# Performance work log

Measured on AMD Instinct MI355X. Metric: run time of the kernel, lower is better.

The kernel has to match this reference:

```python
import jax, jax.numpy as jnp
import numpy as np

KAPPA = 1.0
SIGMA = 0.3
EPS = 1e-5  # torch BatchNorm1d default eps


def _bn(y, g, b):
    # training-mode batch norm: biased batch statistics over the batch axis
    mu = jnp.mean(y, axis=0)
    var = jnp.mean((y - mu) ** 2, axis=0)
    return g * (y - mu) * jax.lax.rsqrt(var + EPS) + b


def _hid(x, W, b, g, be):
    # Linear -> BatchNorm1d -> ReLU
    return jax.nn.relu(_bn(x @ W + b, g, be))


def setup_inputs() -> dict:
    key = jax.random.key(0)
    ks = jax.random.split(key, 12)
    B, D, H, T = 2048, 256, 266, 51  # H = dim + 10
    S = T - 1
    sc = jnp.float32(0.1)
    f32 = jnp.float32
    inp = {}
    inp["x"] = jax.random.normal(ks[0], (B, D), f32)
    inp["dW"] = jax.random.normal(ks[1], (S, B, D), f32)   # hoisted per-step noise xi
    inp["law"] = jax.random.normal(ks[2], (S, D), f32)
    inp["timegrid"] = jnp.linspace(0.0, 1.0, T).astype(f32)
    # per-timestep MLP stacks (i_h1 / h1_h2 / h2_o)
    inp["W1"] = sc * jax.random.normal(ks[3], (S, D, H), f32)
    inp["b1"] = jnp.zeros((S, H), f32)
    inp["g1"] = jnp.ones((S, H), f32)
    inp["be1"] = jnp.zeros((S, H), f32)
    inp["W2"] = sc * jax.random.normal(ks[4], (S, H, H), f32)
    inp["b2"] = jnp.zeros((S, H), f32)
    inp["g2"] = jnp.ones((S, H), f32)
    inp["be2"] = jnp.zeros((S, H), f32)
    inp["W3"] = sc * jax.random.normal(ks[5], (S, H, D), f32)
    inp["b3"] = jnp.zeros((S, D), f32)
    # v0 network (v0_i_h1 / v0_h1_h2 / v0_h2_o, all Linear+BN+ReLU)
    inp["Wv1"] = sc * jax.random.normal(ks[6], (D, H), f32)
    inp["bv1"] = jnp.zeros((H,), f32)
    inp["gv1"] = jnp.ones((H,), f32)
    inp["bev1"] = jnp.zeros((H,), f32)
    inp["Wv2"] = sc * jax.random.normal(ks[7], (H, H), f32)
    inp["bv2"] = jnp.zeros((H,), f32)
    inp["gv2"] = jnp.ones((H,), f32)
    inp["bev2"] = jnp.zeros((H,), f32)
    inp["Wv3"] = sc * jax.random.normal(ks[8], (H, 1), f32)
    inp["bv3"] = jnp.zeros((1,), f32)
    inp["gv3"] = jnp.ones((1,), f32)
    inp["bev3"] = jnp.zeros((1,), f32)
    return inp


def reference(x, dW, law, timegrid,
              W1, b1, g1, be1, W2, b2, g2, be2, W3, b3,
              Wv1, bv1, gv1, bev1, Wv2, bv2, gv2, bev2, Wv3, bv3, gv3, bev3):
    hgrid = jnp.diff(timegrid)  # [S]
    # v0 network evaluated on the initial state (note: last stage is also Linear+BN+ReLU)
    v0 = _hid(_hid(_hid(x, Wv1, bv1, gv1, bev1), Wv2, bv2, gv2, bev2), Wv3, bv3, gv3, bev3)  # [B,1]

    def step(carry, xs):
        xc, v = carry
        w1, bb1, gg1, bbe1, w2, bb2, gg2, bbe2, w3, bb3, li, dw, h = xs
        h1 = _hid(xc, w1, bb1, gg1, bbe1)
        h2 = _hid(h1, w2, bb2, gg2, bbe2)
        grad = h2 @ w3 + bb3                                   # [B,D]
        # f = kappa^2/2 * ||x - law_i||^2 + 1/2 * ||alpha||^2,  alpha = -grad
        f = 0.5 * KAPPA ** 2 * jnp.sum((xc - li) ** 2, axis=1) + 0.5 * jnp.sum(grad ** 2, axis=1)
        noise = SIGMA * jnp.sqrt(h) * dw                       # [B,D]
        # diag(grad @ noise^T) == rowwise dot product: O(B*D) instead of O(B^2*D)
        v = v - (f * h)[:, None] + jnp.sum(grad * noise, axis=1, keepdims=True)
        xc = xc - grad * h + noise
        return (xc, v), None

    (x_final, v), _ = jax.lax.scan(
        step, (x, v0),
        (W1, b1, g1, be1, W2, b2, g2, be2, W3, b3, law, dW, hgrid))
    return v  # [B,1]; (x_final and the path are byproducts of the same scan)
```

## Files before the change

### kernel.cpp

```cpp
#include <hip/hip_runtime.h>
#include <hip/hip_bf16.h>


#define BATCH 2048
#define DD    256
#define HH    266
#define HP    272
#define SS    50
#define BN_EPS 1e-5f
#define SIG   0.3f
#define AS_STRIDE 296
#define YS    276
#define XS    260

#define V_OFF  1638400
#define S1_OFF 1640448
#define S2_OFF 1649152
#define S1V_OFF 1657856
#define S2V_OFF 1662208
#define SV_OFF  1666560
#define WQ_OFF  1666576

#define W1S 69632
#define W2S 78336
#define W3S 73728
#define W1Q_OFF 0
#define W2Q_OFF 3481600
#define W3Q_OFF 7398400
#define WV1Q_OFF 11084800
#define WV2Q_OFF 11154432

#define BAR_OFF 7283200

typedef unsigned short ushort_t;
using short8 = __attribute__((ext_vector_type(8))) short;
using f32x4  = __attribute__((ext_vector_type(4))) float;
using f32x2  = __attribute__((ext_vector_type(2))) float;

__device__ __forceinline__ ushort_t f2b(float f) {
    unsigned u = __float_as_uint(f);
    unsigned r = u + 0x7FFF + ((u >> 16) & 1);
    return (ushort_t)(r >> 16);
}

__device__ __forceinline__ float ld_coh(const float* p) {
    return __hip_atomic_load((const float*)p, __ATOMIC_RELAXED, __HIP_MEMORY_SCOPE_AGENT);
}
__device__ __forceinline__ f32x2 ld2_coh(const float* p) {
    f32x2 v;
    asm volatile("global_load_dwordx2 %0, %1, off sc0 sc1" : "=v"(v) : "v"(p));
    return v;
}

__global__ __launch_bounds__(256) void k_conv(const float* __restrict__ src,
                                              ushort_t* __restrict__ dst,
                                              int K, int N, int KT, int NT,
                                              long total) {
    long t = (long)blockIdx.x * 256 + threadIdx.x;
    if (t >= total) return;
    int per = KT * NT * 512;
    int step = (int)(t / per);
    int e = (int)(t - (long)step * per);
    int kt = e / (NT * 512);
    int r = e - kt * NT * 512;
    int nt = r / 512;
    int r2 = r & 511;
    int lane = r2 >> 3;
    int j = r2 & 7;
    int k = kt * 32 + (lane >> 4) * 8 + j;
    int n = nt * 16 + (lane & 15);
    float v = (k < K && n < N) ? src[(size_t)step * K * N + (size_t)k * N + n] : 0.f;
    dst[t] = f2b(v);
}

__global__ __launch_bounds__(256) void k_pre(float* __restrict__ ws) {
    unsigned* bar = (unsigned*)(ws + BAR_OFF);
    for (int i = threadIdx.x; i < 768; i += 256) atomicExch(bar + i, 0u);
}

__device__ __forceinline__ void grid_bar(unsigned* bar, unsigned gen, int bid) {
    (void)bid;
    __syncthreads();
    if (threadIdx.x == 0) {
        unsigned* cnt = bar;
        unsigned* rel = bar + 32;
        unsigned a = __hip_atomic_fetch_add(cnt, 1u, __ATOMIC_RELAXED, __HIP_MEMORY_SCOPE_AGENT);
        if (a == gen * 128u + 127u) {
            __hip_atomic_store(rel, gen + 1u, __ATOMIC_RELAXED, __HIP_MEMORY_SCOPE_AGENT);
        } else {
            while (__hip_atomic_load(rel, __ATOMIC_RELAXED, __HIP_MEMORY_SCOPE_AGENT) < gen + 1u)
                __builtin_amdgcn_s_sleep(1);
        }
        asm volatile("" ::: "memory");
    }
    __syncthreads();
}

__device__ __forceinline__ void compute_ac_coh(const float* __restrict__ si,
                                               const float* __restrict__ g,
                                               const float* __restrict__ be,
                                               float (*AC)[HP]) {
    int t = threadIdx.x;
    if (t < 136) {
        f32x2 sv[8], qv[8];
        #pragma unroll
        for (int r = 0; r < 8; ++r) {
            sv[r] = ld2_coh(si + r * 544 + 2 * t);
            qv[r] = ld2_coh(si + r * 544 + 272 + 2 * t);
        }
        asm volatile("s_waitcnt vmcnt(0)" ::: "memory");
        __builtin_amdgcn_sched_barrier(0);
        f32x2 s = sv[0], q = qv[0];
        #pragma unroll
        for (int r = 1; r < 8; ++r) { s += sv[r]; q += qv[r]; }
        #pragma unroll
        for (int j = 0; j < 2; ++j) {
            int col = 2 * t + j;
            float a = 0.f, c = 0.f;
            if (col < HH) {
                float mu  = s[j] * (1.0f / 2048.0f);
                float var = q[j] * (1.0f / 2048.0f) - mu * mu;
                float rs  = rsqrtf(fmaxf(var, 0.0f) + BN_EPS);
                a = g[col] * rs;
                c = be[col] - mu * a;
            }
            AC[0][col] = a;
            AC[1][col] = c;
        }
    }
}

__device__ __forceinline__ void dev_lin16(
    int bid, int mode, int KT,
    const float* __restrict__ gsrc, const float* __restrict__ lsrc,
    const float* __restrict__ stats_in, const float* __restrict__ g,
    const float* __restrict__ be,
    const ushort_t* __restrict__ Wq, const float* __restrict__ bias,
    float* __restrict__ ylds, float* __restrict__ stats_out,
    float* __restrict__ zero_ptr,
    const float* __restrict__ pfd, const float* __restrict__ pfl,
    const float* __restrict__ pfb,
    ushort_t* __restrict__ As, float (*AC)[HP])
{
    const int tid  = threadIdx.x;
    const int lane = tid & 63;
    const int wv   = tid >> 6;
    const int quad = lane >> 4;
    const int l15  = lane & 15;
    const int row0 = bid * 16;

    f32x4 pv0 = {0.f,0.f,0.f,0.f}, pv1 = {0.f,0.f,0.f,0.f}, pv2 = {0.f,0.f,0.f,0.f};
    if (pfd != nullptr) {
        pv0 = ((const f32x4*)pfd)[tid];
        pv1 = ((const f32x4*)pfd)[tid + 512];
        if (tid < 64)        pv2 = ((const f32x4*)pfl)[tid];
        else if (tid < 128)  pv2 = ((const f32x4*)pfb)[tid - 64];
    }

    if (zero_ptr != nullptr) {
        int z = bid * 512 + tid;
        if (z < 4352) atomicExch(zero_ptr + z, 0.0f);
    }

    if (mode == 2) { compute_ac_coh(stats_in, g, be, AC); __syncthreads(); }

    const int PAIRS = KT * 16;
    for (int idx = tid; idx < 16 * PAIRS; idx += 512) {
        int m  = idx / PAIRS;
        int kk = (idx - m * PAIRS) * 2;
        float v0, v1;
        if (mode == 2) {
            v0 = (kk < HH)   ? fmaxf(fmaf(AC[0][kk],   lsrc[m * YS + kk],   AC[1][kk]),   0.f) : 0.f;
            v1 = (kk+1 < HH) ? fmaxf(fmaf(AC[0][kk+1], lsrc[m * YS + kk+1], AC[1][kk+1]), 0.f) : 0.f;
        } else {
            v0 = gsrc[(size_t)(row0 + m) * DD + kk];
            v1 = gsrc[(size_t)(row0 + m) * DD + kk + 1];
        }
        ((unsigned int*)As)[m * (AS_STRIDE/2) + (kk >> 1)] =
            (unsigned int)f2b(v0) | ((unsigned int)f2b(v1) << 16);
    }
    if (pfd != nullptr) {
        asm volatile("" :: "v"(pv0), "v"(pv1));
        if (tid < 128) asm volatile("" :: "v"(pv2));
    }
    __syncthreads();

    f32x4 acc[3];
    #pragma unroll
    for (int i = 0; i < 3; ++i) acc[i] = (f32x4){0.f, 0.f, 0.f, 0.f};

    #pragma unroll 3
    for (int kt = 0; kt < KT; ++kt) {
        short8 af = *(const short8*)(&As[l15 * AS_STRIDE + kt * 32 + quad * 8]);
        const ushort_t* wp = Wq + ((size_t)(kt * 17 + wv)) * 512 + lane * 8;
        #pragma unroll
        for (int i = 0; i < 3; ++i) {
            if (i < 2 || wv == 0) {
                short8 bf = *(const short8*)(wp + (size_t)i * 8 * 512);
                acc[i] = __builtin_amdgcn_mfma_f32_16x16x32_bf16(af, bf, acc[i], 0, 0, 0);
            }
        }
    }

    #pragma unroll
    for (int i = 0; i < 3; ++i) {
        if (i == 2 && wv != 0) continue;
        int t = wv + 8 * i;
        int col = t * 16 + l15;
        float bj = (col < HH) ? bias[col] : 0.f;
        float y0 = acc[i][0] + bj, y1 = acc[i][1] + bj;
        float y2 = acc[i][2] + bj, y3 = acc[i][3] + bj;
        ylds[(quad*4 + 0) * YS + col] = y0;
        ylds[(quad*4 + 1) * YS + col] = y1;
        ylds[(quad*4 + 2) * YS + col] = y2;
        ylds[(quad*4 + 3) * YS + col] = y3;
        float sp = y0 + y1 + y2 + y3;
        float sq = y0*y0 + y1*y1 + y2*y2 + y3*y3;
        sp += __shfl_xor(sp, 16); sp += __shfl_xor(sp, 32);
        sq += __shfl_xor(sq, 16); sq += __shfl_xor(sq, 32);
        if (quad == 0 && col < HH) {
            float* spp = stats_out + (bid & 7) * 544;
            atomicAdd(spp + col, sp);
            atomicAdd(spp + 272 + col, sq);
        }
    }
}

__device__ __forceinline__ void dev_fused16(
    int bid,
    const float* __restrict__ y2l, const float* __restrict__ stats_in,
    const float* __restrict__ g2, const float* __restrict__ be2,
    const ushort_t* __restrict__ W3q, const float* __restrict__ b3,
    const float* __restrict__ law, const float* __restrict__ dWs,
    const float* __restrict__ tg, int s, int doP1,
    float* __restrict__ xcl, float* __restrict__ vv, float* __restrict__ outv,
    const ushort_t* __restrict__ W1q, const float* __restrict__ b1n,
    float* __restrict__ y1l, float* __restrict__ stats_out,
    float* __restrict__ zero_ptr,
    ushort_t* __restrict__ As, float (*AC)[HP], float* __restrict__ red)
{
    const int tid  = threadIdx.x;
    const int lane = tid & 63;
    const int wv   = tid >> 6;
    const int quad = lane >> 4;
    const int l15  = lane & 15;
    const int row0 = bid * 16;

    if (zero_ptr != nullptr) {
        int z = bid * 512 + tid;
        if (z < 4352) atomicExch(zero_ptr + z, 0.0f);
    }

    compute_ac_coh(stats_in, g2, be2, AC);
    __syncthreads();

    for (int idx = tid; idx < 16 * 144; idx += 512) {
        int m  = idx / 144;
        int kk = (idx - m * 144) * 2;
        float v0 = (kk < HH)   ? fmaxf(fmaf(AC[0][kk],   y2l[m * YS + kk],   AC[1][kk]),   0.f) : 0.f;
        float v1 = (kk+1 < HH) ? fmaxf(fmaf(AC[0][kk+1], y2l[m * YS + kk+1], AC[1][kk+1]), 0.f) : 0.f;
        ((unsigned int*)As)[m * (AS_STRIDE/2) + (kk >> 1)] =
            (unsigned int)f2b(v0) | ((unsigned int)f2b(v1) << 16);
    }
    __syncthreads();

    f32x4 acc[2];
    acc[0] = (f32x4){0.f,0.f,0.f,0.f};
    acc[1] = (f32x4){0.f,0.f,0.f,0.f};
    #pragma unroll 3
    for (int kt = 0; kt < 9; ++kt) {
        short8 af = *(const short8*)(&As[l15 * AS_STRIDE + kt * 32 + quad * 8]);
        const ushort_t* wp = W3q + ((size_t)(kt * 16 + wv)) * 512 + lane * 8;
        acc[0] = __builtin_amdgcn_mfma_f32_16x16x32_bf16(af, *(const short8*)(wp),           acc[0], 0, 0, 0);
        acc[1] = __builtin_amdgcn_mfma_f32_16x16x32_bf16(af, *(const short8*)(wp + 8 * 512), acc[1], 0, 0, 0);
    }

    const float h   = tg[s + 1] - tg[s];
    const float srt = SIG * sqrtf(h);
    float grad[2][4], xcv[2][4], dwv[2][4];
    float sxr[4], sgr[4], sgnr[4];
    #pragma unroll
    for (int i = 0; i < 2; ++i) {
        int col = (wv + 8*i) * 16 + l15;
        const float lawv = law[col];
        const float b3v  = b3[col];
        #pragma unroll
        for (int r = 0; r < 4; ++r) {
            int rl = quad * 4 + r;
            float gd = acc[i][r] + b3v;
            float xv = xcl[rl * XS + col];
            float dw = dWs[(size_t)(row0 + rl) * DD + col];
            float d  = xv - lawv;
            grad[i][r] = gd; xcv[i][r] = xv; dwv[i][r] = dw;
            if (i == 0) {
                sxr[r]  = d * d;
                sgr[r]  = gd * gd;
                sgnr[r] = gd * dw;
            } else {
                sxr[r]  = fmaf(d, d, sxr[r]);
                sgr[r]  = fmaf(gd, gd, sgr[r]);
                sgnr[r] = fmaf(gd, dw, sgnr[r]);
            }
        }
    }
    #pragma unroll
    for (int off = 1; off < 16; off <<= 1) {
        #pragma unroll
        for (int r = 0; r < 4; ++r) {
            sxr[r]  += __shfl_xor(sxr[r],  off);
            sgr[r]  += __shfl_xor(sgr[r],  off);
            sgnr[r] += __shfl_xor(sgnr[r], off);
        }
    }
    if (l15 == 0) {
        #pragma unroll
        for (int r = 0; r < 4; ++r) {
            int rr = quad * 4 + r;
            red[(wv * 16 + rr) * 3 + 0] = sxr[r];
            red[(wv * 16 + rr) * 3 + 1] = sgr[r];
            red[(wv * 16 + rr) * 3 + 2] = sgnr[r];
        }
    }
    __syncthreads();

    if (tid < 16) {
        float sx = 0.f, sg = 0.f, sgn = 0.f;
        #pragma unroll
        for (int w = 0; w < 8; ++w) {
            sx  += red[(w * 16 + tid) * 3 + 0];
            sg  += red[(w * 16 + tid) * 3 + 1];
            sgn += red[(w * 16 + tid) * 3 + 2];
        }
        int row = row0 + tid;
        float f  = 0.5f * (sx + sg);
        float vn = vv[row] - f * h + srt * sgn;
        vv[row] = vn;
        if (s == SS - 1) outv[row] = vn;
    }

    #pragma unroll
    for (int i = 0; i < 2; ++i) {
        int col = (wv + 8*i) * 16 + l15;
        #pragma unroll
        for (int r = 0; r < 4; ++r) {
            int rl = quad * 4 + r;
            float xn = xcv[i][r] - grad[i][r] * h + srt * dwv[i][r];
            xcl[rl * XS + col] = xn;
            if (doP1) As[rl * AS_STRIDE + col] = f2b(xn);
        }
    }
    if (!doP1) return;
    __syncthreads();

    f32x4 acc2[3];
    #pragma unroll
    for (int i = 0; i < 3; ++i) acc2[i] = (f32x4){0.f, 0.f, 0.f, 0.f};
    #pragma unroll 4
    for (int kt = 0; kt < 8; ++kt) {
        short8 af = *(const short8*)(&As[l15 * AS_STRIDE + kt * 32 + quad * 8]);
        const ushort_t* wp = W1q + ((size_t)(kt * 17 + wv)) * 512 + lane * 8;
        #pragma unroll
        for (int i = 0; i < 3; ++i) {
            if (i < 2 || wv == 0) {
                short8 bf = *(const short8*)(wp + (size_t)i * 8 * 512);
                acc2[i] = __builtin_amdgcn_mfma_f32_16x16x32_bf16(af, bf, acc2[i], 0, 0, 0);
            }
        }
    }
    #pragma unroll
    for (int i = 0; i < 3; ++i) {
        if (i == 2 && wv != 0) continue;
        int t = wv + 8 * i;
        int col = t * 16 + l15;
        float bj = (col < HH) ? b1n[col] : 0.f;
        float y0 = acc2[i][0] + bj, y1 = acc2[i][1] + bj;
        float y2 = acc2[i][2] + bj, y3 = acc2[i][3] + bj;
        y1l[(quad*4 + 0) * YS + col] = y0;
        y1l[(quad*4 + 1) * YS + col] = y1;
        y1l[(quad*4 + 2) * YS + col] = y2;
        y1l[(quad*4 + 3) * YS + col] = y3;
        float sp = y0 + y1 + y2 + y3;
        float sq = y0*y0 + y1*y1 + y2*y2 + y3*y3;
        sp += __shfl_xor(sp, 16); sp += __shfl_xor(sp, 32);
        sq += __shfl_xor(sq, 16); sq += __shfl_xor(sq, 32);
        if (quad == 0 && col < HH) {
            float* spp = stats_out + (bid & 7) * 544;
            atomicAdd(spp + col, sp);
            atomicAdd(spp + 272 + col, sq);
        }
    }
}

__device__ __forceinline__ void dev_v0l3_16(
    int bid, const float* __restrict__ y2l, const float* __restrict__ stats_in,
    const float* __restrict__ gv, const float* __restrict__ bev,
    const float* __restrict__ wv3, const float* __restrict__ bv3,
    float* __restrict__ vout, float* __restrict__ sv,
    float (*AC)[HP], float* __restrict__ xtra)
{
    const int tid = threadIdx.x;
    compute_ac_coh(stats_in, gv, bev, AC);
    __syncthreads();

    const int r  = tid >> 5;
    const int ks = tid & 31;
    int k0 = ks * 9, k1 = k0 + 9;
    if (k1 > HH) k1 = HH;
    float acc = 0.0f;
    for (int k = k0; k < k1; ++k) {
        float y  = y2l[r * YS + k];
        float a2 = fmaxf(fmaf(AC[0][k], y, AC[1][k]), 0.0f);
        acc = fmaf(a2, wv3[k], acc);
    }
    #pragma unroll
    for (int off = 1; off < 32; off <<= 1) acc += __shfl_xor(acc, off);
    if (ks == 0) {
        float y = acc + bv3[0];
        vout[bid * 16 + r] = y;
        xtra[r] = y;
        xtra[16 + r] = y * y;
    }
    __syncthreads();
    if (tid == 0) {
        float s = 0.f, q = 0.f;
        #pragma unroll
        for (int i = 0; i < 16; ++i) { s += xtra[i]; q += xtra[16 + i]; }
        atomicAdd(sv, s);
        atomicAdd(sv + 1, q);
    }
}

__device__ __forceinline__ void dev_v0fin16(int bid, float* __restrict__ v,
                                            const float* __restrict__ sv,
                                            const float* __restrict__ gv3,
                                            const float* __restrict__ bev3) {
    if (threadIdx.x < 16) {
        float s0 = ld_coh(sv);
        float s1 = ld_coh(sv + 1);
        float mu  = s0 * (1.0f / 2048.0f);
        float var = s1 * (1.0f / 2048.0f) - mu * mu;
        float rs  = rsqrtf(fmaxf(var, 0.0f) + BN_EPS);
        int row = bid * 16 + threadIdx.x;
        float y = v[row];
        v[row] = fmaxf(gv3[0] * (y - mu) * rs + bev3[0], 0.0f);
    }
}

__global__ __launch_bounds__(512) void k_persist(
    const float* __restrict__ x, const float* __restrict__ dW,
    const float* __restrict__ law, const float* __restrict__ tg,
    const float* __restrict__ b1, const float* __restrict__ g1, const float* __restrict__ be1,
    const float* __restrict__ b2, const float* __restrict__ g2, const float* __restrict__ be2,
    const float* __restrict__ b3,
    const float* __restrict__ bv1, const float* __restrict__ gv1, const float* __restrict__ bev1,
    const float* __restrict__ bv2, const float* __restrict__ gv2, const float* __restrict__ bev2,
    const float* __restrict__ Wv3, const float* __restrict__ bv3,
    const float* __restrict__ gv3, const float* __restrict__ bev3,
    float* __restrict__ ws, float* __restrict__ out)
{
    __shared__ ushort_t As[16 * AS_STRIDE];
    __shared__ float AC[2][HP];
    __shared__ float Y1s[16 * YS];
    __shared__ float Y2s[16 * YS];
    __shared__ float XCs[16 * XS];
    __shared__ float XTRA[384];

    const int bid = blockIdx.x;
    const int tid = threadIdx.x;

    float* V   = ws + V_OFF;
    float* S1  = ws + S1_OFF;
    float* S2  = ws + S2_OFF;
    float* S1v = ws + S1V_OFF;
    float* S2v = ws + S2V_OFF;
    float* SV  = ws + SV_OFF;
    ushort_t* WQ = (ushort_t*)(ws + WQ_OFF);
    ushort_t* W1q  = WQ + W1Q_OFF;
    ushort_t* W2q  = WQ + W2Q_OFF;
    ushort_t* W3q  = WQ + W3Q_OFF;
    ushort_t* Wv1q = WQ + WV1Q_OFF;
    ushort_t* Wv2q = WQ + WV2Q_OFF;
    unsigned* bar  = (unsigned*)(ws + BAR_OFF);

    unsigned gen = 0;

    for (int i = tid; i < 16 * DD; i += 512) {
        int r = i >> 8, c = i & 255;
        XCs[r * XS + c] = x[(size_t)bid * 16 * DD + i];
    }
    {
        int z = bid * 512 + tid;
        if (z < 26128) atomicExch(S1 + z, 0.0f);
    }
    grid_bar(bar, gen, bid); gen++;

    dev_lin16(bid, 0, 8, x, nullptr, nullptr, nullptr, nullptr,
              Wv1q, bv1, Y1s, S1v, nullptr, nullptr, nullptr, nullptr, As, AC);
    grid_bar(bar, gen, bid); gen++;

    dev_lin16(bid, 2, 9, nullptr, Y1s, S1v, gv1, bev1,
              Wv2q, bv2, Y2s, S2v, nullptr, nullptr, nullptr, nullptr, As, AC);
    grid_bar(bar, gen, bid); gen++;

    dev_v0l3_16(bid, Y2s, S2v, gv2, bev2, Wv3, bv3, V, SV, AC, XTRA);
    grid_bar(bar, gen, bid); gen++;

    dev_v0fin16(bid, V, SV, gv3, bev3);
    dev_lin16(bid, 0, 8, x, nullptr, nullptr, nullptr, nullptr,
              W1q, b1, Y1s, S1, nullptr, nullptr, nullptr, nullptr, As, AC);
    grid_bar(bar, gen, bid); gen++;

    for (int s = 0; s < SS; ++s) {
        int p = s & 1;
        dev_lin16(bid, 2, 9, nullptr, Y1s, S1 + p * 4352,
                  g1 + s * HH, be1 + s * HH,
                  W2q + (size_t)s * W2S, b2 + s * HH,
                  Y2s, S2 + p * 4352, S1 + (1 - p) * 4352,
                  dW + (size_t)s * BATCH * DD + (size_t)bid * 16 * DD,
                  law + (size_t)s * DD, b3 + (size_t)s * DD, As, AC);
        grid_bar(bar, gen, bid); gen++;

        int sn = (s + 1 < SS) ? s + 1 : 0;
        dev_fused16(bid, Y2s, S2 + p * 4352,
                    g2 + s * HH, be2 + s * HH,
                    W3q + (size_t)s * W3S, b3 + s * DD,
                    law + s * DD, dW + (size_t)s * BATCH * DD,
                    tg, s, (s < SS - 1) ? 1 : 0,
                    XCs, V, out,
                    W1q + (size_t)sn * W1S, b1 + sn * HH,
                    Y1s, S1 + ((s + 1) & 1) * 4352,
                    S2 + (1 - p) * 4352, As, AC, XTRA);
        grid_bar(bar, gen, bid); gen++;
    }
}

extern "C" void kernel_launch(void* const* d_in, const int* in_sizes, int n_in,
                              void* d_out, int out_size, void* d_ws, size_t ws_size,
                              hipStream_t stream)
{
    (void)in_sizes; (void)n_in; (void)out_size; (void)ws_size;
    const float* x    = (const float*)d_in[0];
    const float* dW   = (const float*)d_in[1];
    const float* law  = (const float*)d_in[2];
    const float* tg   = (const float*)d_in[3];
    const float* W1   = (const float*)d_in[4];
    const float* b1   = (const float*)d_in[5];
    const float* g1   = (const float*)d_in[6];
    const float* be1  = (const float*)d_in[7];
    const float* W2   = (const float*)d_in[8];
    const float* b2   = (const float*)d_in[9];
    const float* g2   = (const float*)d_in[10];
    const float* be2  = (const float*)d_in[11];
    const float* W3   = (const float*)d_in[12];
    const float* b3   = (const float*)d_in[13];
    const float* Wv1  = (const float*)d_in[14];
    const float* bv1  = (const float*)d_in[15];
    const float* gv1  = (const float*)d_in[16];
    const float* bev1 = (const float*)d_in[17];
    const float* Wv2  = (const float*)d_in[18];
    const float* bv2  = (const float*)d_in[19];
    const float* gv2  = (const float*)d_in[20];
    const float* bev2 = (const float*)d_in[21];
    const float* Wv3  = (const float*)d_in[22];
    const float* bv3  = (const float*)d_in[23];
    const float* gv3  = (const float*)d_in[24];
    const float* bev3 = (const float*)d_in[25];

    float* ws = (float*)d_ws;
    ushort_t* WQ = (ushort_t*)(ws + WQ_OFF);
    ushort_t* W1q  = WQ + W1Q_OFF;
    ushort_t* W2q  = WQ + W2Q_OFF;
    ushort_t* W3q  = WQ + W3Q_OFF;
    ushort_t* Wv1q = WQ + WV1Q_OFF;
    ushort_t* Wv2q = WQ + WV2Q_OFF;
    float* out = (float*)d_out;

    k_pre<<<1, 256, 0, stream>>>(ws);
    k_conv<<<13600, 256, 0, stream>>>(W1,  W1q,  DD, HH, 8, 17, (long)SS * W1S);
    k_conv<<<15300, 256, 0, stream>>>(W2,  W2q,  HH, HH, 9, 17, (long)SS * W2S);
    k_conv<<<14400, 256, 0, stream>>>(W3,  W3q,  HH, DD, 9, 16, (long)SS * W3S);
    k_conv<<<272,   256, 0, stream>>>(Wv1, Wv1q, DD, HH, 8, 17, (long)W1S);
    k_conv<<<306,   256, 0, stream>>>(Wv2, Wv2q, HH, HH, 9, 17, (long)W2S);

    k_persist<<<128, 512, 0, stream>>>(
        x, dW, law, tg,
        b1, g1, be1, b2, g2, be2, b3,
        bv1, gv1, bev1, bv2, gv2, bev2,
        Wv3, bv3, gv3, bev3,
        ws, out);
}
```

Baseline: 1.458 ms.

## Use hierarchical grid barrier and prefetch next-stage weights before barriers

Replaces the single-counter grid barrier with a two-level tree: 8 leaf counters of 16 blocks each, a root counter, and per-leaf release flags, so the 128 blocks no longer contend on one atomic. Prefetches move to just before each barrier and now cover the block's 16-row slice of dW, law and b3, plus a 1/16 slice of the next W3, W1 and W2 bf16 weights, to warm L2 while blocks wait. Zeroing of the stats buffers is spread as small per-block chunks instead of being done by the first few blocks. The gain depends on barrier latency and L2 hit rates, and the two-level barrier adds an extra atomic hop on the critical path.

```diff
diff --git a/kernel.cpp b/kernel.cpp
--- a/kernel.cpp
+++ b/kernel.cpp
@@ -50,6 +50,13 @@
     f32x2 v;
     asm volatile("global_load_dwordx2 %0, %1, off sc0 sc1" : "=v"(v) : "v"(p));
     return v;
+}
+__device__ __forceinline__ void pf2(const f32x4* q, int n, int tid,
+                                    f32x4& r0, f32x4& r1) {
+    int i0 = (tid < n) ? tid : 0;
+    int i1 = (tid + 512 < n) ? (tid + 512) : 0;
+    r0 = q[i0];
+    r1 = q[i1];
 }
 
 __global__ __launch_bounds__(256) void k_conv(const float* __restrict__ src,
@@ -79,15 +86,24 @@
 }
 
 __device__ __forceinline__ void grid_bar(unsigned* bar, unsigned gen, int bid) {
-    (void)bid;
     __syncthreads();
     if (threadIdx.x == 0) {
-        unsigned* cnt = bar;
-        unsigned* rel = bar + 32;
-        unsigned a = __hip_atomic_fetch_add(cnt, 1u, __ATOMIC_RELAXED, __HIP_MEMORY_SCOPE_AGENT);
-        if (a == gen * 128u + 127u) {
-            __hip_atomic_store(rel, gen + 1u, __ATOMIC_RELAXED, __HIP_MEMORY_SCOPE_AGENT);
-        } else {
+        const int lf = bid & 7;
+        unsigned* leaf = bar + lf * 32;
+        unsigned* root = bar + 256;
+        unsigned* rel  = bar + 288 + lf * 32;
+        bool done = false;
+        unsigned a = __hip_atomic_fetch_add(leaf, 1u, __ATOMIC_RELAXED, __HIP_MEMORY_SCOPE_AGENT);
+        if (a == gen * 16u + 15u) {
+            unsigned r = __hip_atomic_fetch_add(root, 1u, __ATOMIC_RELAXED, __HIP_MEMORY_SCOPE_AGENT);
+            if (r == gen * 8u + 7u) {
+                #pragma unroll
+                for (int l = 0; l < 8; ++l)
+                    __hip_atomic_store(bar + 288 + l * 32, gen + 1u, __ATOMIC_RELAXED, __HIP_MEMORY_SCOPE_AGENT);
+                done = true;
+            }
+        }
+        if (!done) {
             while (__hip_atomic_load(rel, __ATOMIC_RELAXED, __HIP_MEMORY_SCOPE_AGENT) < gen + 1u)
                 __builtin_amdgcn_s_sleep(1);
         }
@@ -138,8 +154,6 @@
     const ushort_t* __restrict__ Wq, const float* __restrict__ bias,
     float* __restrict__ ylds, float* __restrict__ stats_out,
     float* __restrict__ zero_ptr,
-    const float* __restrict__ pfd, const float* __restrict__ pfl,
-    const float* __restrict__ pfb,
     ushort_t* __restrict__ As, float (*AC)[HP])
 {
     const int tid  = threadIdx.x;
@@ -149,18 +163,8 @@
     const int l15  = lane & 15;
     const int row0 = bid * 16;
 
-    f32x4 pv0 = {0.f,0.f,0.f,0.f}, pv1 = {0.f,0.f,0.f,0.f}, pv2 = {0.f,0.f,0.f,0.f};
-    if (pfd != nullptr) {
-        pv0 = ((const f32x4*)pfd)[tid];
-        pv1 = ((const f32x4*)pfd)[tid + 512];
-        if (tid < 64)        pv2 = ((const f32x4*)pfl)[tid];
-        else if (tid < 128)  pv2 = ((const f32x4*)pfb)[tid - 64];
-    }
-
-    if (zero_ptr != nullptr) {
-        int z = bid * 512 + tid;
-        if (z < 4352) atomicExch(zero_ptr + z, 0.0f);
-    }
+    if (zero_ptr != nullptr && tid < 34)
+        atomicExch(zero_ptr + bid * 34 + tid, 0.0f);
 
     if (mode == 2) { compute_ac_coh(stats_in, g, be, AC); __syncthreads(); }
 
@@ -178,10 +182,6 @@
         }
         ((unsigned int*)As)[m * (AS_STRIDE/2) + (kk >> 1)] =
             (unsigned int)f2b(v0) | ((unsigned int)f2b(v1) << 16);
-    }
-    if (pfd != nullptr) {
-        asm volatile("" :: "v"(pv0), "v"(pv1));
-        if (tid < 128) asm volatile("" :: "v"(pv2));
     }
     __syncthreads();
 
@@ -246,10 +246,8 @@
     const int l15  = lane & 15;
     const int row0 = bid * 16;
 
-    if (zero_ptr != nullptr) {
-        int z = bid * 512 + tid;
-        if (z < 4352) atomicExch(zero_ptr + z, 0.0f);
-    }
+    if (zero_ptr != nullptr && tid < 34)
+        atomicExch(zero_ptr + bid * 34 + tid, 0.0f);
 
     compute_ac_coh(stats_in, g2, be2, AC);
     __syncthreads();
@@ -483,23 +481,25 @@
     unsigned* bar  = (unsigned*)(ws + BAR_OFF);
 
     unsigned gen = 0;
+    const int sl = (bid >> 3) & 15;
 
     for (int i = tid; i < 16 * DD; i += 512) {
         int r = i >> 8, c = i & 255;
         XCs[r * XS + c] = x[(size_t)bid * 16 * DD + i];
     }
     {
-        int z = bid * 512 + tid;
-        if (z < 26128) atomicExch(S1 + z, 0.0f);
+        int z = bid * 205 + tid;
+        int ze = (bid + 1) * 205; if (ze > 26128) ze = 26128;
+        if (tid < 205 && z < ze) atomicExch(S1 + z, 0.0f);
     }
     grid_bar(bar, gen, bid); gen++;
 
     dev_lin16(bid, 0, 8, x, nullptr, nullptr, nullptr, nullptr,
-              Wv1q, bv1, Y1s, S1v, nullptr, nullptr, nullptr, nullptr, As, AC);
+              Wv1q, bv1, Y1s, S1v, nullptr, As, AC);
     grid_bar(bar, gen, bid); gen++;
 
     dev_lin16(bid, 2, 9, nullptr, Y1s, S1v, gv1, bev1,
-              Wv2q, bv2, Y2s, S2v, nullptr, nullptr, nullptr, nullptr, As, AC);
+              Wv2q, bv2, Y2s, S2v, nullptr, As, AC);
     grid_bar(bar, gen, bid); gen++;
 
     dev_v0l3_16(bid, Y2s, S2v, gv2, bev2, Wv3, bv3, V, SV, AC, XTRA);
@@ -507,7 +507,12 @@
 
     dev_v0fin16(bid, V, SV, gv3, bev3);
     dev_lin16(bid, 0, 8, x, nullptr, nullptr, nullptr, nullptr,
-              W1q, b1, Y1s, S1, nullptr, nullptr, nullptr, nullptr, As, AC);
+              W1q, b1, Y1s, S1, nullptr, As, AC);
+    {
+        f32x4 p0, p1;
+        pf2((const f32x4*)((const char*)W2q + (size_t)sl * 9792), 612, tid, p0, p1);
+        asm volatile("" :: "v"(p0), "v"(p1));
+    }
     grid_bar(bar, gen, bid); gen++;
 
     for (int s = 0; s < SS; ++s) {
@@ -515,9 +520,22 @@
         dev_lin16(bid, 2, 9, nullptr, Y1s, S1 + p * 4352,
                   g1 + s * HH, be1 + s * HH,
                   W2q + (size_t)s * W2S, b2 + s * HH,
-                  Y2s, S2 + p * 4352, S1 + (1 - p) * 4352,
-                  dW + (size_t)s * BATCH * DD + (size_t)bid * 16 * DD,
-                  law + (size_t)s * DD, b3 + (size_t)s * DD, As, AC);
+                  Y2s, S2 + p * 4352, S1 + (1 - p) * 4352, As, AC);
+        {
+            f32x4 d0, d1, w30, w31, w10, w11, lb;
+            pf2((const f32x4*)(dW + (size_t)s * BATCH * DD + (size_t)bid * 16 * DD),
+                1024, tid, d0, d1);
+            pf2((const f32x4*)((const char*)(W3q + (size_t)s * W3S) + (size_t)sl * 9216),
+                576, tid, w30, w31);
+            int sn0 = (s + 1 < SS) ? s + 1 : s;
+            pf2((const f32x4*)((const char*)(W1q + (size_t)sn0 * W1S) + (size_t)sl * 8704),
+                544, tid, w10, w11);
+            const f32x4* ql = (const f32x4*)(law + (size_t)s * DD);
+            const f32x4* qb = (const f32x4*)(b3 + (size_t)s * DD);
+            lb = (tid < 64) ? ql[tid] : ((tid < 128) ? qb[tid - 64] : ql[0]);
+            asm volatile("" :: "v"(d0), "v"(d1), "v"(w30), "v"(w31),
+                              "v"(w10), "v"(w11), "v"(lb));
+        }
         grid_bar(bar, gen, bid); gen++;
 
         int sn = (s + 1 < SS) ? s + 1 : 0;
@@ -530,6 +548,12 @@
                     W1q + (size_t)sn * W1S, b1 + sn * HH,
                     Y1s, S1 + ((s + 1) & 1) * 4352,
                     S2 + (1 - p) * 4352, As, AC, XTRA);
+        if (s + 1 < SS) {
+            f32x4 p0, p1;
+            pf2((const f32x4*)((const char*)(W2q + (size_t)(s + 1) * W2S) + (size_t)sl * 9792),
+                612, tid, p0, p1);
+            asm volatile("" :: "v"(p0), "v"(p1));
+        }
         grid_bar(bar, gen, bid); gen++;
     }
 }
```

Result: faster. 1.233 ms (-15.4%).
